# Performance work log

Measured on AMD Instinct MI355X. Metric: run time of the kernel, lower is better.

## Reference

```python
import jax, jax.numpy as jnp
import numpy as np

OUT_F, IN_F = 4096, 4096
BITS = 4
B, S = 4, 2048


def setup_inputs() -> dict:
    key = jax.random.key(0)
    k_x, k_cb, k_rot, k_b, k_idx = jax.random.split(key, 5)
    x = jax.random.normal(k_x, (B, S, IN_F), dtype=jnp.float32)
    # per-coordinate codebook indices for each weight row (int, constant)
    indices = jax.random.randint(k_idx, (OUT_F, IN_F), 0, 2 ** BITS, dtype=jnp.int32)
    # scalar codebook with 2^bits levels
    codebook = jax.random.normal(k_cb, (2 ** BITS,), dtype=jnp.float32)
    # random rotation Pi (d x d); faithful math only needs it orthogonal-ish
    rotation_matrix = jax.random.normal(k_rot, (IN_F, IN_F), dtype=jnp.float32) / np.sqrt(IN_F)
    bias = jax.random.normal(k_b, (OUT_F,), dtype=jnp.float32)
    return {"x": x, "indices": indices, "codebook": codebook,
            "rotation_matrix": rotation_matrix, "bias": bias}


def reference(x, indices, codebook, rotation_matrix, bias):
    # Dequantize: look up codewords per coordinate in rotated space, then
    # undo the rotation: W = C[idx] @ Pi^T  -> [out_features, in_features]
    rotated = codebook[indices]                      # [O, D] gather
    weight = jnp.einsum('od,kd->ok', rotated, rotation_matrix)  # rotated @ Pi^T
    # F.linear(x, W, bias) = x @ W^T + bias
    out = jnp.einsum('bsd,od->bso', x, weight) + bias
    return out
```

## Files before the change

### kernel.cpp

```cpp
#include <hip/hip_runtime.h>
#include <hip/hip_bf16.h>


typedef __attribute__((ext_vector_type(8))) __bf16 bf16x8;
typedef __attribute__((ext_vector_type(4))) float f32x4;

#define GLOAD_LDS16(g, l)                                                        \
  __builtin_amdgcn_global_load_lds((__attribute__((address_space(1))) void*)(g), \
                                   (__attribute__((address_space(3))) void*)(l), \
                                   16, 0, 0)


__global__ __launch_bounds__(256) void cvt_f32_bf16(const float* __restrict__ in,
                                                    __hip_bfloat16* __restrict__ out, int n4) {
  int i = blockIdx.x * 256 + threadIdx.x;
  if (i >= n4) return;
  float4 v = *(const float4*)(in + (size_t)i * 4);
  union { __hip_bfloat16 h[4]; ushort4 u; } o;
  o.h[0] = __float2bfloat16(v.x);
  o.h[1] = __float2bfloat16(v.y);
  o.h[2] = __float2bfloat16(v.z);
  o.h[3] = __float2bfloat16(v.w);
  *(ushort4*)((unsigned short*)out + (size_t)i * 4) = o.u;
}

__global__ __launch_bounds__(256) void dequant_bf16(const int* __restrict__ idx,
                                                    const float* __restrict__ cb,
                                                    __hip_bfloat16* __restrict__ out, int n4) {
  __shared__ __hip_bfloat16 scb[16];
  if (threadIdx.x < 16) scb[threadIdx.x] = __float2bfloat16(cb[threadIdx.x]);
  __syncthreads();
  int i = blockIdx.x * 256 + threadIdx.x;
  if (i >= n4) return;
  int4 v = *(const int4*)(idx + (size_t)i * 4);
  union { __hip_bfloat16 h[4]; ushort4 u; } o;
  o.h[0] = scb[v.x & 15];
  o.h[1] = scb[v.y & 15];
  o.h[2] = scb[v.z & 15];
  o.h[3] = scb[v.w & 15];
  *(ushort4*)((unsigned short*)out + (size_t)i * 4) = o.u;
}


template <bool OUT_BF16>
__global__ __launch_bounds__(512, 2) void gemm256(const __hip_bfloat16* __restrict__ A,
                                                  const __hip_bfloat16* __restrict__ B,
                                                  void* __restrict__ Cv,
                                                  const float* __restrict__ bias,
                                                  int M, int N, int K) {
  __shared__ __align__(16) char smem[131072];

  const int nbn = N >> 8;
  const int nwg = (M >> 8) * nbn;
  const int bid0 = blockIdx.x;
  const int cpx = nwg >> 3;
  const int bid = (bid0 & 7) * cpx + (bid0 >> 3);
  const int m0 = (bid / nbn) << 8;
  const int n0 = (bid % nbn) << 8;

  const int tid = (int)threadIdx.x;
  const int lane = tid & 63;
  const int w = tid >> 6;
  const int wr = w >> 2;
  const int wc = w & 3;
  const int fr = lane & 15;
  const int fq = lane >> 4;

  const int srow = lane >> 3;
  const int scol = ((lane & 7) ^ srow) << 3;

  const __hip_bfloat16* Ab = A + (size_t)m0 * K;
  const __hip_bfloat16* Bb = B + (size_t)n0 * K;

  const int NT = K >> 6;

  f32x4 acc[8][4];
#pragma unroll
  for (int i = 0; i < 8; ++i)
#pragma unroll
    for (int j = 0; j < 4; ++j) acc[i][j] = (f32x4){0.f, 0.f, 0.f, 0.f};

  auto stage = [&](int s) {
    const int t = s >> 2, kind = s & 3;
    const __hip_bfloat16* g = (kind < 2) ? Ab : Bb;
    char* region = smem + ((kind < 2) ? 0 : 65536) + (t & 1) * 32768 + (kind & 1) * 16384;
    const int grow = (kind & 1) * 128 + w * 16 + srow;
    const int k0 = t << 6;
#pragma unroll
    for (int j = 0; j < 2; ++j)
      GLOAD_LDS16(g + (size_t)(grow + j * 8) * K + (k0 + scol), region + w * 2048 + j * 1024);
  };

  const int sw = (fr & 7) << 4;

  auto ldA = [&](int b, int mh, int mf, int kk) -> bf16x8 {
    const int row = wr * 128 + mh * 64 + mf * 16 + fr;
    const int byte = b * 32768 + row * 128 + ((kk * 64 + fq * 16) ^ sw);
    return *(const bf16x8*)(smem + byte);
  };
  auto ldB = [&](int b, int nh, int nf, int kk) -> bf16x8 {
    const int row = wc * 64 + nh * 32 + nf * 16 + fr;
    const int byte = 65536 + b * 32768 + row * 128 + ((kk * 64 + fq * 16) ^ sw);
    return *(const bf16x8*)(smem + byte);
  };

#pragma unroll
  for (int s = 0; s < 5; ++s) stage(s);
  asm volatile("s_waitcnt vmcnt(2)");
  __builtin_amdgcn_s_barrier();

  bf16x8 af[4][2], b0[2][2], b1[2][2];

  for (int T = 0; T < NT; ++T) {
    const int b = T & 1;
#pragma unroll
    for (int mf = 0; mf < 4; ++mf)
#pragma unroll
      for (int kk = 0; kk < 2; ++kk) af[mf][kk] = ldA(b, 0, mf, kk);
#pragma unroll
    for (int nf = 0; nf < 2; ++nf)
#pragma unroll
      for (int kk = 0; kk < 2; ++kk) b0[nf][kk] = ldB(b, 0, nf, kk);
    if (T + 1 < NT) stage(4 * T + 5);
    __builtin_amdgcn_s_barrier();
    asm volatile("s_waitcnt lgkmcnt(0)");
    __builtin_amdgcn_sched_barrier(0);
    __builtin_amdgcn_s_setprio(1);
#pragma unroll
    for (int mf = 0; mf < 4; ++mf)
#pragma unroll
      for (int nf = 0; nf < 2; ++nf)
#pragma unroll
        for (int kk = 0; kk < 2; ++kk)
          acc[mf][nf] =
              __builtin_amdgcn_mfma_f32_16x16x32_bf16(af[mf][kk], b0[nf][kk], acc[mf][nf], 0, 0, 0);
    __builtin_amdgcn_s_setprio(0);
    __builtin_amdgcn_s_barrier();

#pragma unroll
    for (int nf = 0; nf < 2; ++nf)
#pragma unroll
      for (int kk = 0; kk < 2; ++kk) b1[nf][kk] = ldB(b, 1, nf, kk);
    if (T + 1 < NT) stage(4 * T + 6);
    __builtin_amdgcn_s_barrier();
    asm volatile("s_waitcnt lgkmcnt(0)");
    __builtin_amdgcn_sched_barrier(0);
    __builtin_amdgcn_s_setprio(1);
#pragma unroll
    for (int mf = 0; mf < 4; ++mf)
#pragma unroll
      for (int nf = 0; nf < 2; ++nf)
#pragma unroll
        for (int kk = 0; kk < 2; ++kk)
          acc[mf][2 + nf] = __builtin_amdgcn_mfma_f32_16x16x32_bf16(af[mf][kk], b1[nf][kk],
                                                                    acc[mf][2 + nf], 0, 0, 0);
    __builtin_amdgcn_s_setprio(0);
    __builtin_amdgcn_s_barrier();

#pragma unroll
    for (int mf = 0; mf < 4; ++mf)
#pragma unroll
      for (int kk = 0; kk < 2; ++kk) af[mf][kk] = ldA(b, 1, mf, kk);
    if (T + 1 < NT) stage(4 * T + 7);
    __builtin_amdgcn_s_barrier();
    asm volatile("s_waitcnt lgkmcnt(0)");
    __builtin_amdgcn_sched_barrier(0);
    __builtin_amdgcn_s_setprio(1);
#pragma unroll
    for (int mf = 0; mf < 4; ++mf)
#pragma unroll
      for (int nf = 0; nf < 2; ++nf)
#pragma unroll
        for (int kk = 0; kk < 2; ++kk)
          acc[4 + mf][2 + nf] = __builtin_amdgcn_mfma_f32_16x16x32_bf16(
              af[mf][kk], b1[nf][kk], acc[4 + mf][2 + nf], 0, 0, 0);
    __builtin_amdgcn_s_setprio(0);
    __builtin_amdgcn_s_barrier();

    if (T + 2 < NT) stage(4 * T + 8);
    __builtin_amdgcn_s_barrier();
    __builtin_amdgcn_s_setprio(1);
#pragma unroll
    for (int mf = 0; mf < 4; ++mf)
#pragma unroll
      for (int nf = 0; nf < 2; ++nf)
#pragma unroll
        for (int kk = 0; kk < 2; ++kk)
          acc[4 + mf][nf] = __builtin_amdgcn_mfma_f32_16x16x32_bf16(af[mf][kk], b0[nf][kk],
                                                                    acc[4 + mf][nf], 0, 0, 0);
    __builtin_amdgcn_s_setprio(0);
    if (T + 2 < NT) {
      asm volatile("s_waitcnt vmcnt(2)");
    } else if (T + 2 == NT) {
      asm volatile("s_waitcnt vmcnt(0)");
    }
    __builtin_amdgcn_s_barrier();
  }

  if constexpr (OUT_BF16) {
    __hip_bfloat16* C = (__hip_bfloat16*)Cv;
#pragma unroll
    for (int mi = 0; mi < 8; ++mi)
#pragma unroll
      for (int ni = 0; ni < 4; ++ni) {
        const size_t row = (size_t)(m0 + wr * 128 + (mi >> 2) * 64 + (mi & 3) * 16 + fq * 4);
        const int col = n0 + wc * 64 + (ni >> 1) * 32 + (ni & 1) * 16 + fr;
#pragma unroll
        for (int v = 0; v < 4; ++v) C[(row + v) * N + col] = __float2bfloat16(acc[mi][ni][v]);
      }
  } else {
    float* C = (float*)Cv;
    float bv[4];
#pragma unroll
    for (int ni = 0; ni < 4; ++ni)
      bv[ni] = bias[n0 + wc * 64 + (ni >> 1) * 32 + (ni & 1) * 16 + fr];
#pragma unroll
    for (int mi = 0; mi < 8; ++mi)
#pragma unroll
      for (int ni = 0; ni < 4; ++ni) {
        const size_t row = (size_t)(m0 + wr * 128 + (mi >> 2) * 64 + (mi & 3) * 16 + fq * 4);
        const int col = n0 + wc * 64 + (ni >> 1) * 32 + (ni & 1) * 16 + fr;
#pragma unroll
        for (int v = 0; v < 4; ++v) C[(row + v) * N + col] = acc[mi][ni][v] + bv[ni];
      }
  }
}


extern "C" void kernel_launch(void* const* d_in, const int* in_sizes, int n_in,
                              void* d_out, int out_size, void* d_ws, size_t ws_size,
                              hipStream_t stream) {
  const float* x = (const float*)d_in[0];
  const int* indices = (const int*)d_in[1];
  const float* codebook = (const float*)d_in[2];
  const float* rot = (const float*)d_in[3];
  const float* bias = (const float*)d_in[4];
  float* out = (float*)d_out;

  const int D = 4096, O = 4096;
  const int M = in_sizes[0] / D;

  char* ws = (char*)d_ws;
  __hip_bfloat16* Xb = (__hip_bfloat16*)ws;
  __hip_bfloat16* Rb = (__hip_bfloat16*)(ws + ((size_t)64 << 20));
  __hip_bfloat16* Wr = (__hip_bfloat16*)(ws + ((size_t)96 << 20));
  __hip_bfloat16* Wb = (__hip_bfloat16*)(ws + ((size_t)128 << 20));

  cvt_f32_bf16<<<(M * D / 4 + 255) / 256, 256, 0, stream>>>(x, Xb, M * D / 4);
  cvt_f32_bf16<<<(4096 * 4096 / 4 + 255) / 256, 256, 0, stream>>>(rot, Rb, 4096 * 4096 / 4);
  dequant_bf16<<<(4096 * 4096 / 4 + 255) / 256, 256, 0, stream>>>(indices, codebook, Wr,
                                                                  4096 * 4096 / 4);

  gemm256<true><<<dim3((O / 256) * (4096 / 256)), 512, 0, stream>>>(Wr, Rb, Wb, nullptr, O, 4096,
                                                                    D);
  gemm256<false><<<dim3((M / 256) * (O / 256)), 512, 0, stream>>>(Xb, Wb, out, bias, M, O, 4096);
}
```

Measured before the change: 444.2 us.

## Deepen GEMM global-to-LDS prefetch to two tiles ahead

Reworks the software pipeline of the bf16 GEMM so global_load_lds stages for tile T+2 are issued during tile T, with all eight stages preloaded in the prologue. The old scheme issued loads for the next tile's partial regions interleaved per quarter. Waits change to vmcnt(8), keeping more loads in flight to hide global memory latency. It relies on the LDS buffer layout allowing the reuse ordering; a mismatch could race or read stale data.

Result: no change. 450.3 us (+1.4%).

```diff
diff --git a/kernel.cpp b/kernel.cpp
--- a/kernel.cpp
+++ b/kernel.cpp
@@ -105,14 +105,17 @@
   };
 
 #pragma unroll
-  for (int s = 0; s < 5; ++s) stage(s);
-  asm volatile("s_waitcnt vmcnt(2)");
+  for (int s = 0; s < 8; ++s) stage(s);
+  __builtin_amdgcn_sched_barrier(0);
+  asm volatile("s_waitcnt vmcnt(8)" ::: "memory");
+  __builtin_amdgcn_sched_barrier(0);
   __builtin_amdgcn_s_barrier();
 
   bf16x8 af[4][2], b0[2][2], b1[2][2];
 
   for (int T = 0; T < NT; ++T) {
     const int b = T & 1;
+    const bool pf = (T + 2 < NT);
 #pragma unroll
     for (int mf = 0; mf < 4; ++mf)
 #pragma unroll
@@ -121,9 +124,8 @@
     for (int nf = 0; nf < 2; ++nf)
 #pragma unroll
       for (int kk = 0; kk < 2; ++kk) b0[nf][kk] = ldB(b, 0, nf, kk);
-    if (T + 1 < NT) stage(4 * T + 5);
-    __builtin_amdgcn_s_barrier();
-    asm volatile("s_waitcnt lgkmcnt(0)");
+    __builtin_amdgcn_s_barrier();
+    asm volatile("s_waitcnt lgkmcnt(0)" ::: "memory");
     __builtin_amdgcn_sched_barrier(0);
     __builtin_amdgcn_s_setprio(1);
 #pragma unroll
@@ -141,9 +143,8 @@
     for (int nf = 0; nf < 2; ++nf)
 #pragma unroll
       for (int kk = 0; kk < 2; ++kk) b1[nf][kk] = ldB(b, 1, nf, kk);
-    if (T + 1 < NT) stage(4 * T + 6);
-    __builtin_amdgcn_s_barrier();
-    asm volatile("s_waitcnt lgkmcnt(0)");
+    __builtin_amdgcn_s_barrier();
+    asm volatile("s_waitcnt lgkmcnt(0)" ::: "memory");
     __builtin_amdgcn_sched_barrier(0);
     __builtin_amdgcn_s_setprio(1);
 #pragma unroll
@@ -161,9 +162,12 @@
     for (int mf = 0; mf < 4; ++mf)
 #pragma unroll
       for (int kk = 0; kk < 2; ++kk) af[mf][kk] = ldA(b, 1, mf, kk);
-    if (T + 1 < NT) stage(4 * T + 7);
-    __builtin_amdgcn_s_barrier();
-    asm volatile("s_waitcnt lgkmcnt(0)");
+    if (pf) {
+      stage(4 * (T + 2) + 2);
+      stage(4 * (T + 2) + 3);
+    }
+    __builtin_amdgcn_s_barrier();
+    asm volatile("s_waitcnt lgkmcnt(0)" ::: "memory");
     __builtin_amdgcn_sched_barrier(0);
     __builtin_amdgcn_s_setprio(1);
 #pragma unroll
@@ -177,7 +181,10 @@
     __builtin_amdgcn_s_setprio(0);
     __builtin_amdgcn_s_barrier();
 
-    if (T + 2 < NT) stage(4 * T + 8);
+    if (pf) {
+      stage(4 * (T + 2) + 0);
+      stage(4 * (T + 2) + 1);
+    }
     __builtin_amdgcn_s_barrier();
     __builtin_amdgcn_s_setprio(1);
 #pragma unroll
@@ -189,11 +196,13 @@
           acc[4 + mf][nf] = __builtin_amdgcn_mfma_f32_16x16x32_bf16(af[mf][kk], b0[nf][kk],
                                                                     acc[4 + mf][nf], 0, 0, 0);
     __builtin_amdgcn_s_setprio(0);
-    if (T + 2 < NT) {
-      asm volatile("s_waitcnt vmcnt(2)");
+    __builtin_amdgcn_sched_barrier(0);
+    if (pf) {
+      asm volatile("s_waitcnt vmcnt(8)" ::: "memory");
     } else if (T + 2 == NT) {
-      asm volatile("s_waitcnt vmcnt(0)");
+      asm volatile("s_waitcnt vmcnt(0)" ::: "memory");
     }
+    __builtin_amdgcn_sched_barrier(0);
     __builtin_amdgcn_s_barrier();
   }
 
```

## Restructure GEMM main loop to split K-halves across phases with reordered staging

Applied to the files above, without the earlier changes.

Reorganizes the per-tile loop so each phase consumes one 32-wide K slice for a full 64x64 (or half) subtile instead of splitting by N halves, loading all B fragments for a K slice once and reusing them across both M halves. The global-to-LDS stage order changes: the two B K-halves of the next tile are prefetched two tiles ahead while A is prefetched one ahead, and wait counts are adjusted to vmcnt(4). It is meant to cut LDS fragment reloads and register pressure (fewer live bf16x8 registers) and to give more overlap between loads and MFMAs. It risks LDS buffer hazards if the new stage ordering is wrong.

Measured after the change: 441.2 us. About the same (-0.7%).

```diff
diff --git a/kernel.cpp b/kernel.cpp
--- a/kernel.cpp
+++ b/kernel.cpp
@@ -98,101 +98,94 @@
     const int byte = b * 32768 + row * 128 + ((kk * 64 + fq * 16) ^ sw);
     return *(const bf16x8*)(smem + byte);
   };
-  auto ldB = [&](int b, int nh, int nf, int kk) -> bf16x8 {
-    const int row = wc * 64 + nh * 32 + nf * 16 + fr;
+  auto ldB = [&](int b, int nf, int kk) -> bf16x8 {
+    const int row = wc * 64 + nf * 16 + fr;
     const int byte = 65536 + b * 32768 + row * 128 + ((kk * 64 + fq * 16) ^ sw);
     return *(const bf16x8*)(smem + byte);
   };
 
-#pragma unroll
-  for (int s = 0; s < 5; ++s) stage(s);
-  asm volatile("s_waitcnt vmcnt(2)");
+  stage(0); stage(1); stage(2); stage(3);
+  stage(6); stage(7);
+  asm volatile("s_waitcnt vmcnt(4)" ::: "memory");
   __builtin_amdgcn_s_barrier();
 
-  bf16x8 af[4][2], b0[2][2], b1[2][2];
+  bf16x8 af0[4], af1[4], bfr[4][2];
 
   for (int T = 0; T < NT; ++T) {
     const int b = T & 1;
-#pragma unroll
-    for (int mf = 0; mf < 4; ++mf)
-#pragma unroll
-      for (int kk = 0; kk < 2; ++kk) af[mf][kk] = ldA(b, 0, mf, kk);
-#pragma unroll
-    for (int nf = 0; nf < 2; ++nf)
-#pragma unroll
-      for (int kk = 0; kk < 2; ++kk) b0[nf][kk] = ldB(b, 0, nf, kk);
-    if (T + 1 < NT) stage(4 * T + 5);
-    __builtin_amdgcn_s_barrier();
-    asm volatile("s_waitcnt lgkmcnt(0)");
-    __builtin_amdgcn_sched_barrier(0);
-    __builtin_amdgcn_s_setprio(1);
-#pragma unroll
-    for (int mf = 0; mf < 4; ++mf)
-#pragma unroll
-      for (int nf = 0; nf < 2; ++nf)
-#pragma unroll
-        for (int kk = 0; kk < 2; ++kk)
-          acc[mf][nf] =
-              __builtin_amdgcn_mfma_f32_16x16x32_bf16(af[mf][kk], b0[nf][kk], acc[mf][nf], 0, 0, 0);
-    __builtin_amdgcn_s_setprio(0);
-    __builtin_amdgcn_s_barrier();
-
-#pragma unroll
-    for (int nf = 0; nf < 2; ++nf)
-#pragma unroll
-      for (int kk = 0; kk < 2; ++kk) b1[nf][kk] = ldB(b, 1, nf, kk);
-    if (T + 1 < NT) stage(4 * T + 6);
-    __builtin_amdgcn_s_barrier();
-    asm volatile("s_waitcnt lgkmcnt(0)");
-    __builtin_amdgcn_sched_barrier(0);
-    __builtin_amdgcn_s_setprio(1);
-#pragma unroll
-    for (int mf = 0; mf < 4; ++mf)
-#pragma unroll
-      for (int nf = 0; nf < 2; ++nf)
-#pragma unroll
-        for (int kk = 0; kk < 2; ++kk)
-          acc[mf][2 + nf] = __builtin_amdgcn_mfma_f32_16x16x32_bf16(af[mf][kk], b1[nf][kk],
-                                                                    acc[mf][2 + nf], 0, 0, 0);
-    __builtin_amdgcn_s_setprio(0);
-    __builtin_amdgcn_s_barrier();
-
-#pragma unroll
-    for (int mf = 0; mf < 4; ++mf)
-#pragma unroll
-      for (int kk = 0; kk < 2; ++kk) af[mf][kk] = ldA(b, 1, mf, kk);
-    if (T + 1 < NT) stage(4 * T + 7);
-    __builtin_amdgcn_s_barrier();
-    asm volatile("s_waitcnt lgkmcnt(0)");
-    __builtin_amdgcn_sched_barrier(0);
-    __builtin_amdgcn_s_setprio(1);
-#pragma unroll
-    for (int mf = 0; mf < 4; ++mf)
-#pragma unroll
-      for (int nf = 0; nf < 2; ++nf)
-#pragma unroll
-        for (int kk = 0; kk < 2; ++kk)
-          acc[4 + mf][2 + nf] = __builtin_amdgcn_mfma_f32_16x16x32_bf16(
-              af[mf][kk], b1[nf][kk], acc[4 + mf][2 + nf], 0, 0, 0);
-    __builtin_amdgcn_s_setprio(0);
-    __builtin_amdgcn_s_barrier();
-
-    if (T + 2 < NT) stage(4 * T + 8);
-    __builtin_amdgcn_s_barrier();
-    __builtin_amdgcn_s_setprio(1);
-#pragma unroll
-    for (int mf = 0; mf < 4; ++mf)
-#pragma unroll
-      for (int nf = 0; nf < 2; ++nf)
-#pragma unroll
-        for (int kk = 0; kk < 2; ++kk)
-          acc[4 + mf][nf] = __builtin_amdgcn_mfma_f32_16x16x32_bf16(af[mf][kk], b0[nf][kk],
-                                                                    acc[4 + mf][nf], 0, 0, 0);
-    __builtin_amdgcn_s_setprio(0);
-    if (T + 2 < NT) {
-      asm volatile("s_waitcnt vmcnt(2)");
+    const bool pf1 = (T + 1 < NT);
+    const bool pf2 = (T + 2 < NT);
+
+#pragma unroll
+    for (int mf = 0; mf < 4; ++mf) af0[mf] = ldA(b, 0, mf, 0);
+#pragma unroll
+    for (int nf = 0; nf < 4; ++nf) bfr[nf][0] = ldB(b, nf, 0);
+    if (pf1) stage(4 * (T + 1) + 0);
+    __builtin_amdgcn_s_barrier();
+    asm volatile("s_waitcnt lgkmcnt(0)");
+    __builtin_amdgcn_sched_barrier(0);
+    __builtin_amdgcn_s_setprio(1);
+#pragma unroll
+    for (int nf = 0; nf < 4; ++nf)
+#pragma unroll
+      for (int mf = 0; mf < 4; ++mf)
+        acc[mf][nf] =
+            __builtin_amdgcn_mfma_f32_16x16x32_bf16(af0[mf], bfr[nf][0], acc[mf][nf], 0, 0, 0);
+    __builtin_amdgcn_s_setprio(0);
+    __builtin_amdgcn_s_barrier();
+
+#pragma unroll
+    for (int mf = 0; mf < 4; ++mf) af1[mf] = ldA(b, 0, mf, 1);
+#pragma unroll
+    for (int nf = 0; nf < 4; ++nf) bfr[nf][1] = ldB(b, nf, 1);
+    if (pf1) stage(4 * (T + 1) + 1);
+    __builtin_amdgcn_s_barrier();
+    asm volatile("s_waitcnt lgkmcnt(0)");
+    __builtin_amdgcn_sched_barrier(0);
+    __builtin_amdgcn_s_setprio(1);
+#pragma unroll
+    for (int nf = 0; nf < 4; ++nf)
+#pragma unroll
+      for (int mf = 0; mf < 4; ++mf)
+        acc[mf][nf] =
+            __builtin_amdgcn_mfma_f32_16x16x32_bf16(af1[mf], bfr[nf][1], acc[mf][nf], 0, 0, 0);
+    __builtin_amdgcn_s_setprio(0);
+    __builtin_amdgcn_s_barrier();
+
+#pragma unroll
+    for (int mf = 0; mf < 4; ++mf) af0[mf] = ldA(b, 1, mf, 0);
+    if (pf2) stage(4 * (T + 2) + 2);
+    __builtin_amdgcn_s_barrier();
+    asm volatile("s_waitcnt lgkmcnt(0)");
+    __builtin_amdgcn_sched_barrier(0);
+    __builtin_amdgcn_s_setprio(1);
+#pragma unroll
+    for (int nf = 0; nf < 4; ++nf)
+#pragma unroll
+      for (int mf = 0; mf < 4; ++mf)
+        acc[4 + mf][nf] =
+            __builtin_amdgcn_mfma_f32_16x16x32_bf16(af0[mf], bfr[nf][0], acc[4 + mf][nf], 0, 0, 0);
+    __builtin_amdgcn_s_setprio(0);
+    __builtin_amdgcn_s_barrier();
+
+#pragma unroll
+    for (int mf = 0; mf < 4; ++mf) af1[mf] = ldA(b, 1, mf, 1);
+    if (pf2) stage(4 * (T + 2) + 3);
+    __builtin_amdgcn_s_barrier();
+    asm volatile("s_waitcnt lgkmcnt(0)");
+    __builtin_amdgcn_sched_barrier(0);
+    __builtin_amdgcn_s_setprio(1);
+#pragma unroll
+    for (int nf = 0; nf < 4; ++nf)
+#pragma unroll
+      for (int mf = 0; mf < 4; ++mf)
+        acc[4 + mf][nf] =
+            __builtin_amdgcn_mfma_f32_16x16x32_bf16(af1[mf], bfr[nf][1], acc[4 + mf][nf], 0, 0, 0);
+    __builtin_amdgcn_s_setprio(0);
+    if (pf2) {
+      asm volatile("s_waitcnt vmcnt(4)" ::: "memory");
     } else if (T + 2 == NT) {
-      asm volatile("s_waitcnt vmcnt(0)");
+      asm volatile("s_waitcnt vmcnt(0)" ::: "memory");
     }
     __builtin_amdgcn_s_barrier();
   }
@@ -204,7 +197,7 @@
 #pragma unroll
       for (int ni = 0; ni < 4; ++ni) {
         const size_t row = (size_t)(m0 + wr * 128 + (mi >> 2) * 64 + (mi & 3) * 16 + fq * 4);
-        const int col = n0 + wc * 64 + (ni >> 1) * 32 + (ni & 1) * 16 + fr;
+        const int col = n0 + wc * 64 + ni * 16 + fr;
 #pragma unroll
         for (int v = 0; v < 4; ++v) C[(row + v) * N + col] = __float2bfloat16(acc[mi][ni][v]);
       }
@@ -212,14 +205,13 @@
     float* C = (float*)Cv;
     float bv[4];
 #pragma unroll
-    for (int ni = 0; ni < 4; ++ni)
-      bv[ni] = bias[n0 + wc * 64 + (ni >> 1) * 32 + (ni & 1) * 16 + fr];
+    for (int ni = 0; ni < 4; ++ni) bv[ni] = bias[n0 + wc * 64 + ni * 16 + fr];
 #pragma unroll
     for (int mi = 0; mi < 8; ++mi)
 #pragma unroll
       for (int ni = 0; ni < 4; ++ni) {
         const size_t row = (size_t)(m0 + wr * 128 + (mi >> 2) * 64 + (mi & 3) * 16 + fq * 4);
-        const int col = n0 + wc * 64 + (ni >> 1) * 32 + (ni & 1) * 16 + fr;
+        const int col = n0 + wc * 64 + ni * 16 + fr;
 #pragma unroll
         for (int v = 0; v < 4; ++v) C[(row + v) * N + col] = acc[mi][ni][v] + bv[ni];
       }
```
